# Performance work log

Measured on AMD Instinct MI355X. Metric: run time of the kernel, lower is better.

## Reference

```python
import jax, jax.numpy as jnp
import numpy as np

ALPHA = 0.2  # leaky-relu negative slope AND the residual scale self.alpha

def setup_inputs() -> dict:
    key = jax.random.key(0)
    k1, k2, k3 = jax.random.split(key, 3)
    B, N, C_in, C_out = 8, 2048, 128, 128
    text = jax.random.normal(k1, (B, N, C_in), dtype=jnp.float32)
    adj = jnp.ones((B, N, N), dtype=jnp.float32)  # unused by the layer's forward
    W = jax.random.normal(k2, (C_in, C_out), dtype=jnp.float32) * (1.414 / np.sqrt(C_in + C_out))
    a = jax.random.normal(k3, (2 * C_out, 1), dtype=jnp.float32) * (1.414 / np.sqrt(2 * C_out + 1))
    return {"text": text, "adj": adj, "W": W, "a": a}

def reference(text, adj, W, a):
    # text: [B,N,C_in]; adj is unused (faithful to the source forward).
    h = jnp.einsum('bnc,cf->bnf', text, W)                  # [B,N,F]
    F_out = W.shape[1]
    a1 = a[:F_out, 0]                                       # score contribution of node i
    a2 = a[F_out:, 0]                                       # score contribution of node j
    s1 = jnp.einsum('bnf,f->bn', h, a1)                     # [B,N]
    s2 = jnp.einsum('bnf,f->bn', h, a2)                     # [B,N]
    # leakyrelu(cat(h_i,h_j) @ a) == leakyrelu(s1_i + s2_j): avoids O(N^2*2F) concat
    e = jax.nn.leaky_relu(s1[:, :, None] + s2[:, None, :], negative_slope=ALPHA)  # [B,N,N]
    attention = jax.nn.softmax(e, axis=2)                   # dropout is a no-op in eval mode
    h_prime = jnp.einsum('bij,bjf->bif', attention, h)      # [B,N,F]
    return jax.nn.elu(h_prime + ALPHA * h)
```

## Files before the change

kernel.cpp:

```cpp
#include <hip/hip_runtime.h>
#include <hip/hip_bf16.h>
#include <math.h>

#define LRELU_ALPHA 0.2f

constexpr int B_ = 8;
constexpr int N_ = 2048;
constexpr int M_ = B_ * N_;
constexpr int SEG = 32;
constexpr int NSEG = N_ / SEG;

__global__ __launch_bounds__(256) void k_gemm(const float* __restrict__ text,
                                              const float* __restrict__ W,
                                              const float* __restrict__ a,
                                              float* __restrict__ h,
                                              float* __restrict__ s1,
                                              float* __restrict__ s2,
                                              float* __restrict__ eN0,
                                              float* __restrict__ eP0) {
    __shared__ __align__(16) float As[64 * 132];

    const int tid = threadIdx.x;
    const int r0  = blockIdx.x * 64;
    const int cx  = tid & 15;
    const int ry  = tid >> 4;
    const int c0  = cx * 4;
    const int c1  = 64 + cx * 4;
    const int rr0 = ry * 4;

    for (int idx = tid; idx < 64 * 32; idx += 256) {
        int r = idx >> 5, k4 = (idx & 31) * 4;
        *(float4*)&As[r * 132 + k4] =
            *(const float4*)&text[(size_t)(r0 + r) * 128 + k4];
    }
    __syncthreads();

    float acc[4][8];
#pragma unroll
    for (int i = 0; i < 4; ++i)
#pragma unroll
        for (int j = 0; j < 8; ++j) acc[i][j] = 0.f;

#pragma unroll 2
    for (int k0 = 0; k0 < 128; k0 += 4) {
        float4 av[4];
#pragma unroll
        for (int i = 0; i < 4; ++i)
            av[i] = *(const float4*)&As[(rr0 + i) * 132 + k0];
#pragma unroll
        for (int kk = 0; kk < 4; ++kk) {
            float4 w0 = *(const float4*)&W[(size_t)(k0 + kk) * 128 + c0];
            float4 w1 = *(const float4*)&W[(size_t)(k0 + kk) * 128 + c1];
#pragma unroll
            for (int i = 0; i < 4; ++i) {
                const float avv = (kk == 0) ? av[i].x : (kk == 1) ? av[i].y
                                : (kk == 2) ? av[i].z : av[i].w;
                acc[i][0] += avv * w0.x; acc[i][1] += avv * w0.y;
                acc[i][2] += avv * w0.z; acc[i][3] += avv * w0.w;
                acc[i][4] += avv * w1.x; acc[i][5] += avv * w1.y;
                acc[i][6] += avv * w1.z; acc[i][7] += avv * w1.w;
            }
        }
    }

    float4 a1lo = *(const float4*)&a[c0];
    float4 a1hi = *(const float4*)&a[c1];
    float4 a2lo = *(const float4*)&a[128 + c0];
    float4 a2hi = *(const float4*)&a[128 + c1];

#pragma unroll
    for (int i = 0; i < 4; ++i) {
        const int row = r0 + rr0 + i;
        float4 o0 = {acc[i][0], acc[i][1], acc[i][2], acc[i][3]};
        float4 o1 = {acc[i][4], acc[i][5], acc[i][6], acc[i][7]};
        *(float4*)&h[(size_t)row * 128 + c0] = o0;
        *(float4*)&h[(size_t)row * 128 + c1] = o1;

        float p1 = o0.x*a1lo.x + o0.y*a1lo.y + o0.z*a1lo.z + o0.w*a1lo.w
                 + o1.x*a1hi.x + o1.y*a1hi.y + o1.z*a1hi.z + o1.w*a1hi.w;
        float p2 = o0.x*a2lo.x + o0.y*a2lo.y + o0.z*a2lo.z + o0.w*a2lo.w
                 + o1.x*a2hi.x + o1.y*a2hi.y + o1.z*a2hi.z + o1.w*a2hi.w;
#pragma unroll
        for (int off = 8; off >= 1; off >>= 1) {
            p1 += __shfl_xor(p1, off);
            p2 += __shfl_xor(p2, off);
        }
        if (cx == 0) {
            s1[row] = p1;
            s2[row] = p2;
            eN0[row] = expf(LRELU_ALPHA * p2);
            eP0[row] = expf(p2);
        }
    }
}

__global__ __launch_bounds__(512) void k_rank(const float* __restrict__ s2,
                                              const float* __restrict__ eN0,
                                              const float* __restrict__ eP0,
                                              const float* __restrict__ s1,
                                              int* __restrict__ perm,
                                              float* __restrict__ eNs,
                                              float* __restrict__ ePs,
                                              int* __restrict__ rank,
                                              float* __restrict__ ZN,
                                              float* __restrict__ ZP) {
    __shared__ float ls2[2048], leN[2048], leP[2048];
    __shared__ int   redc[512], redm[512];
    __shared__ float redn[512], redp[512];

    const int b  = blockIdx.x >> 5;
    const int eb = blockIdx.x & 31;
    const int tid = threadIdx.x;
    const int e = tid & 63;
    const int c = tid >> 6;

    {
        const float4* g2 = (const float4*)(s2  + b * 2048);
        const float4* gn = (const float4*)(eN0 + b * 2048);
        const float4* gp = (const float4*)(eP0 + b * 2048);
        ((float4*)ls2)[tid] = g2[tid];
        ((float4*)leN)[tid] = gn[tid];
        ((float4*)leP)[tid] = gp[tid];
    }
    __syncthreads();

    const int i  = eb * 64 + e;
    const int gi = b * 2048 + i;
    const float myS2 = ls2[i];
    const float thr  = -s1[gi];

    int cnt = 0, mr = 0;
    float sn = 0.f, sp = 0.f;
    const int j0 = c * 256;
#pragma unroll 4
    for (int j = j0; j < j0 + 256; j += 4) {
        float4 v  = *(const float4*)&ls2[j];
        float4 en = *(const float4*)&leN[j];
        float4 ep = *(const float4*)&leP[j];
#define PROC(vv, ee, pp, jj)                                             \
        { bool le = (vv) <= thr;                                         \
          cnt += le ? 1 : 0;                                             \
          sn  += le ? (ee) : 0.f;                                        \
          sp  += le ? 0.f : (pp);                                        \
          mr  += ((vv) < myS2 || ((vv) == myS2 && (jj) < i)) ? 1 : 0; }
        PROC(v.x, en.x, ep.x, j + 0)
        PROC(v.y, en.y, ep.y, j + 1)
        PROC(v.z, en.z, ep.z, j + 2)
        PROC(v.w, en.w, ep.w, j + 3)
#undef PROC
    }
    redc[tid] = cnt; redm[tid] = mr; redn[tid] = sn; redp[tid] = sp;
    __syncthreads();
    if (c == 0) {
        int tc = 0, tm = 0; float tn = 0.f, tp = 0.f;
#pragma unroll
        for (int cc = 0; cc < 8; ++cc) {
            tc += redc[cc * 64 + e];
            tm += redm[cc * 64 + e];
            tn += redn[cc * 64 + e];
            tp += redp[cc * 64 + e];
        }
        perm[b * 2048 + tm] = i;
        eNs [b * 2048 + tm] = leN[i];
        ePs [b * 2048 + tm] = leP[i];
        rank[gi] = tc;
        ZN[gi] = tn;
        ZP[gi] = tp;
    }
}

__global__ __launch_bounds__(128) void k_segsum(const float* __restrict__ h,
                                                const int* __restrict__ perm,
                                                const float* __restrict__ eNs,
                                                const float* __restrict__ ePs,
                                                float* __restrict__ segN,
                                                float* __restrict__ segP) {
    const int blk = blockIdx.x;
    const int b = blk >> 6, s = blk & 63;
    const int f = threadIdx.x;
    const int rbase = s * SEG;
    float an = 0.f, ap = 0.f;
#pragma unroll 4
    for (int r = 0; r < SEG; ++r) {
        int rr = b * 2048 + rbase + r;
        float hv = h[(size_t)(b * 2048 + perm[rr]) * 128 + f];
        an += eNs[rr] * hv;
        ap += ePs[rr] * hv;
    }
    segN[blk * 128 + f] = an;
    segP[blk * 128 + f] = ap;
}

__global__ __launch_bounds__(128) void k_prefix(const float* __restrict__ h,
                                                const int* __restrict__ perm,
                                                const float* __restrict__ eNs,
                                                const float* __restrict__ ePs,
                                                const float* __restrict__ segN,
                                                const float* __restrict__ segP,
                                                __hip_bfloat16* __restrict__ Pre,
                                                __hip_bfloat16* __restrict__ Suf) {
    const int blk  = blockIdx.x;
    const int dir  = blk & 1;
    const int task = blk >> 1;
    const int b = task >> 6, s = task & 63;
    const int f = threadIdx.x;
    const int rbase = s * SEG;

    if (dir == 0) {
        float an = 0.f;
        for (int ss = 0; ss < s; ++ss) an += segN[(b * NSEG + ss) * 128 + f];
#pragma unroll 4
        for (int r = 0; r < SEG; ++r) {
            int rr = b * 2048 + rbase + r;
            Pre[(size_t)(b * 2049 + rbase + r) * 128 + f] = __float2bfloat16(an);
            an += eNs[rr] * h[(size_t)(b * 2048 + perm[rr]) * 128 + f];
        }
        if (s == NSEG - 1)
            Pre[(size_t)(b * 2049 + 2048) * 128 + f] = __float2bfloat16(an);
    } else {
        float ap = 0.f;
        for (int ss = s + 1; ss < NSEG; ++ss) ap += segP[(b * NSEG + ss) * 128 + f];
#pragma unroll 4
        for (int r = SEG - 1; r >= 0; --r) {
            int rr = b * 2048 + rbase + r;
            ap += ePs[rr] * h[(size_t)(b * 2048 + perm[rr]) * 128 + f];
            Suf[(size_t)(b * 2049 + rbase + r) * 128 + f] = __float2bfloat16(ap);
        }
        if (s == NSEG - 1)
            Suf[(size_t)(b * 2049 + 2048) * 128 + f] = __float2bfloat16(0.f);
    }
}

__global__ __launch_bounds__(256) void k_out(const float* __restrict__ h,
                                             const float* __restrict__ s1,
                                             const int* __restrict__ rank,
                                             const float* __restrict__ ZN,
                                             const float* __restrict__ ZP,
                                             const __hip_bfloat16* __restrict__ Pre,
                                             const __hip_bfloat16* __restrict__ Suf,
                                             float* __restrict__ out) {
    const int tid = threadIdx.x;
    const int lr = tid >> 7, f = tid & 127;
    const int i = blockIdx.x * 2 + lr;
    const int b = i >> 11;

    const float s1v = s1[i];
    const float E1 = expf(s1v);
    const float E2 = expf(LRELU_ALPHA * s1v);
    const int   r  = rank[i];
    const float Z  = E1 * ZP[i] + E2 * ZN[i];
    const size_t o = (size_t)(b * 2049 + r) * 128 + f;
    const float hp = (E1 * __bfloat162float(Suf[o]) + E2 * __bfloat162float(Pre[o])) / Z;
    const float x = hp + LRELU_ALPHA * h[(size_t)i * 128 + f];
    out[(size_t)i * 128 + f] = (x > 0.f) ? x : expm1f(x);
}

extern "C" void kernel_launch(void* const* d_in, const int* in_sizes, int n_in,
                              void* d_out, int out_size, void* d_ws, size_t ws_size,
                              hipStream_t stream) {
    const float* text = (const float*)d_in[0];
    const float* W = (const float*)d_in[2];
    const float* a = (const float*)d_in[3];
    float* out = (float*)d_out;

    float* p = (float*)d_ws;
    float* h    = p; p += (size_t)M_ * 128;
    float* s1   = p; p += M_;
    float* s2   = p; p += M_;
    float* eN0  = p; p += M_;
    float* eP0  = p; p += M_;
    int*   perm = (int*)p; p += M_;
    float* eNs  = p; p += M_;
    float* ePs  = p; p += M_;
    int*   rank = (int*)p; p += M_;
    float* ZN   = p; p += M_;
    float* ZP   = p; p += M_;
    float* segN = p; p += B_ * NSEG * 128;
    float* segP = p; p += B_ * NSEG * 128;
    __hip_bfloat16* Pre = (__hip_bfloat16*)p; p += (size_t)B_ * 2049 * 128 / 2;
    __hip_bfloat16* Suf = (__hip_bfloat16*)p; p += (size_t)B_ * 2049 * 128 / 2;

    hipLaunchKernelGGL(k_gemm,   dim3(M_ / 64),       dim3(256), 0, stream,
                       text, W, a, h, s1, s2, eN0, eP0);
    hipLaunchKernelGGL(k_rank,   dim3(B_ * 32),       dim3(512), 0, stream,
                       s2, eN0, eP0, s1, perm, eNs, ePs, rank, ZN, ZP);
    hipLaunchKernelGGL(k_segsum, dim3(B_ * NSEG),     dim3(128), 0, stream,
                       h, perm, eNs, ePs, segN, segP);
    hipLaunchKernelGGL(k_prefix, dim3(B_ * NSEG * 2), dim3(128), 0, stream,
                       h, perm, eNs, ePs, segN, segP, Pre, Suf);
    hipLaunchKernelGGL(k_out,    dim3(M_ / 2),        dim3(256), 0, stream,
                       h, s1, rank, ZN, ZP, Pre, Suf, out);
}
```

Baseline: 267.7 us.

## Fuse prefix scan and output into bucketed per-segment kernel, stage W in LDS

Merges the prefix/suffix scan and output kernels into one kernel per segment. It keeps the scanned prefix and suffix rows in shared memory instead of writing bf16 Pre/Suf arrays to global memory. Nodes are bucketed by rank segment with atomics in the rank kernel so each block can emit the outputs whose rank falls in its segment. The GEMM now stages W in LDS, and the h gathers in segsum and scan are hoisted into registers. Risks include a serial per-bucket output loop with uneven bucket sizes, and extra LDS use in the GEMM that may lower occupancy.

```diff
diff --git a/kernel.cpp b/kernel.cpp
--- a/kernel.cpp
+++ b/kernel.cpp
@@ -17,11 +17,18 @@
                                               float* __restrict__ s1,
                                               float* __restrict__ s2,
                                               float* __restrict__ eN0,
-                                              float* __restrict__ eP0) {
+                                              float* __restrict__ eP0,
+                                              int* __restrict__ bcnt) {
     __shared__ __align__(16) float As[64 * 132];
+    __shared__ __align__(16) float Ws[128 * 128];
 
     const int tid = threadIdx.x;
-    const int r0  = blockIdx.x * 64;
+    const int blk = blockIdx.x;
+
+    if (blk == 0)
+        for (int t = tid; t < B_ * NSEG; t += 256) bcnt[t] = 0;
+
+    const int r0  = blk * 64;
     const int cx  = tid & 15;
     const int ry  = tid >> 4;
     const int c0  = cx * 4;
@@ -33,6 +40,10 @@
         *(float4*)&As[r * 132 + k4] =
             *(const float4*)&text[(size_t)(r0 + r) * 128 + k4];
     }
+    for (int idx = tid; idx < 128 * 32; idx += 256) {
+        int k = idx >> 5, f4 = (idx & 31) * 4;
+        *(float4*)&Ws[k * 128 + f4] = *(const float4*)&W[(size_t)k * 128 + f4];
+    }
     __syncthreads();
 
     float acc[4][8];
@@ -49,8 +60,8 @@
             av[i] = *(const float4*)&As[(rr0 + i) * 132 + k0];
 #pragma unroll
         for (int kk = 0; kk < 4; ++kk) {
-            float4 w0 = *(const float4*)&W[(size_t)(k0 + kk) * 128 + c0];
-            float4 w1 = *(const float4*)&W[(size_t)(k0 + kk) * 128 + c1];
+            float4 w0 = *(const float4*)&Ws[(k0 + kk) * 128 + c0];
+            float4 w1 = *(const float4*)&Ws[(k0 + kk) * 128 + c1];
 #pragma unroll
             for (int i = 0; i < 4; ++i) {
                 const float avv = (kk == 0) ? av[i].x : (kk == 1) ? av[i].y
@@ -101,9 +112,10 @@
                                               int* __restrict__ perm,
                                               float* __restrict__ eNs,
                                               float* __restrict__ ePs,
-                                              int* __restrict__ rank,
                                               float* __restrict__ ZN,
-                                              float* __restrict__ ZP) {
+                                              float* __restrict__ ZP,
+                                              int* __restrict__ bcnt,
+                                              int* __restrict__ bucket) {
     __shared__ float ls2[2048], leN[2048], leP[2048];
     __shared__ int   redc[512], redm[512];
     __shared__ float redn[512], redp[512];
@@ -163,9 +175,12 @@
         perm[b * 2048 + tm] = i;
         eNs [b * 2048 + tm] = leN[i];
         ePs [b * 2048 + tm] = leP[i];
-        rank[gi] = tc;
         ZN[gi] = tn;
         ZP[gi] = tp;
+        const int seg = min(tc >> 5, NSEG - 1);
+        const int pos = atomicAdd(&bcnt[b * NSEG + seg], 1);
+        if (pos < 2048)
+            bucket[(b * NSEG + seg) * 2048 + pos] = i | (tc << 11);
     }
 }
 
@@ -178,81 +193,87 @@
     const int blk = blockIdx.x;
     const int b = blk >> 6, s = blk & 63;
     const int f = threadIdx.x;
-    const int rbase = s * SEG;
+    const int rr0 = b * 2048 + s * SEG;
+
+    int pm[SEG];
+#pragma unroll
+    for (int r = 0; r < SEG; ++r) pm[r] = perm[rr0 + r];
+    float hv[SEG];
+#pragma unroll
+    for (int r = 0; r < SEG; ++r)
+        hv[r] = h[(size_t)(b * 2048 + pm[r]) * 128 + f];
+
     float an = 0.f, ap = 0.f;
-#pragma unroll 4
+#pragma unroll
     for (int r = 0; r < SEG; ++r) {
-        int rr = b * 2048 + rbase + r;
-        float hv = h[(size_t)(b * 2048 + perm[rr]) * 128 + f];
-        an += eNs[rr] * hv;
-        ap += ePs[rr] * hv;
+        an += eNs[rr0 + r] * hv[r];
+        ap += ePs[rr0 + r] * hv[r];
     }
     segN[blk * 128 + f] = an;
     segP[blk * 128 + f] = ap;
 }
 
-__global__ __launch_bounds__(128) void k_prefix(const float* __restrict__ h,
-                                                const int* __restrict__ perm,
-                                                const float* __restrict__ eNs,
-                                                const float* __restrict__ ePs,
-                                                const float* __restrict__ segN,
-                                                const float* __restrict__ segP,
-                                                __hip_bfloat16* __restrict__ Pre,
-                                                __hip_bfloat16* __restrict__ Suf) {
-    const int blk  = blockIdx.x;
-    const int dir  = blk & 1;
-    const int task = blk >> 1;
-    const int b = task >> 6, s = task & 63;
+__global__ __launch_bounds__(128) void k_scanout(
+    const float* __restrict__ h, const int* __restrict__ perm,
+    const float* __restrict__ eNs, const float* __restrict__ ePs,
+    const float* __restrict__ s1,
+    const float* __restrict__ ZN, const float* __restrict__ ZP,
+    const float* __restrict__ segN, const float* __restrict__ segP,
+    const int* __restrict__ bcnt, const int* __restrict__ bucket,
+    float* __restrict__ out) {
+
+    __shared__ float anL[(SEG + 1) * 128];
+    __shared__ float apL[(SEG + 1) * 128];
+
+    const int blk = blockIdx.x;
+    const int b = blk >> 6, s = blk & 63;
     const int f = threadIdx.x;
-    const int rbase = s * SEG;
-
-    if (dir == 0) {
-        float an = 0.f;
-        for (int ss = 0; ss < s; ++ss) an += segN[(b * NSEG + ss) * 128 + f];
-#pragma unroll 4
-        for (int r = 0; r < SEG; ++r) {
-            int rr = b * 2048 + rbase + r;
-            Pre[(size_t)(b * 2049 + rbase + r) * 128 + f] = __float2bfloat16(an);
-            an += eNs[rr] * h[(size_t)(b * 2048 + perm[rr]) * 128 + f];
-        }
-        if (s == NSEG - 1)
-            Pre[(size_t)(b * 2049 + 2048) * 128 + f] = __float2bfloat16(an);
-    } else {
-        float ap = 0.f;
-        for (int ss = s + 1; ss < NSEG; ++ss) ap += segP[(b * NSEG + ss) * 128 + f];
-#pragma unroll 4
-        for (int r = SEG - 1; r >= 0; --r) {
-            int rr = b * 2048 + rbase + r;
-            ap += ePs[rr] * h[(size_t)(b * 2048 + perm[rr]) * 128 + f];
-            Suf[(size_t)(b * 2049 + rbase + r) * 128 + f] = __float2bfloat16(ap);
-        }
-        if (s == NSEG - 1)
-            Suf[(size_t)(b * 2049 + 2048) * 128 + f] = __float2bfloat16(0.f);
-    }
-}
-
-__global__ __launch_bounds__(256) void k_out(const float* __restrict__ h,
-                                             const float* __restrict__ s1,
-                                             const int* __restrict__ rank,
-                                             const float* __restrict__ ZN,
-                                             const float* __restrict__ ZP,
-                                             const __hip_bfloat16* __restrict__ Pre,
-                                             const __hip_bfloat16* __restrict__ Suf,
-                                             float* __restrict__ out) {
-    const int tid = threadIdx.x;
-    const int lr = tid >> 7, f = tid & 127;
-    const int i = blockIdx.x * 2 + lr;
-    const int b = i >> 11;
-
-    const float s1v = s1[i];
-    const float E1 = expf(s1v);
-    const float E2 = expf(LRELU_ALPHA * s1v);
-    const int   r  = rank[i];
-    const float Z  = E1 * ZP[i] + E2 * ZN[i];
-    const size_t o = (size_t)(b * 2049 + r) * 128 + f;
-    const float hp = (E1 * __bfloat162float(Suf[o]) + E2 * __bfloat162float(Pre[o])) / Z;
-    const float x = hp + LRELU_ALPHA * h[(size_t)i * 128 + f];
-    out[(size_t)i * 128 + f] = (x > 0.f) ? x : expm1f(x);
+
+    float bn = 0.f, bp = 0.f;
+    for (int ss = 0; ss < s; ++ss)        bn += segN[(b * NSEG + ss) * 128 + f];
+    for (int ss = s + 1; ss < NSEG; ++ss) bp += segP[(b * NSEG + ss) * 128 + f];
+
+    const int rr0 = b * 2048 + s * SEG;
+    int pm[SEG];
+#pragma unroll
+    for (int r = 0; r < SEG; ++r) pm[r] = perm[rr0 + r];
+    float hv[SEG];
+#pragma unroll
+    for (int r = 0; r < SEG; ++r)
+        hv[r] = h[(size_t)(b * 2048 + pm[r]) * 128 + f];
+
+    float an = bn;
+#pragma unroll
+    for (int r = 0; r < SEG; ++r) {
+        anL[r * 128 + f] = an;
+        an += eNs[rr0 + r] * hv[r];
+    }
+    anL[SEG * 128 + f] = an;
+
+    float ap = bp;
+    apL[SEG * 128 + f] = ap;
+#pragma unroll
+    for (int r = SEG - 1; r >= 0; --r) {
+        ap += ePs[rr0 + r] * hv[r];
+        apL[r * 128 + f] = ap;
+    }
+    __syncthreads();
+
+    const int m = min(bcnt[b * NSEG + s], 2048);
+    for (int t = 0; t < m; ++t) {
+        const int packed = bucket[(b * NSEG + s) * 2048 + t];
+        const int il = packed & 2047;
+        const int tc = packed >> 11;
+        const int gi = b * 2048 + il;
+        const int pl = tc - s * SEG;
+        const float s1v = s1[gi];
+        const float E1 = expf(s1v);
+        const float E2 = expf(LRELU_ALPHA * s1v);
+        const float Z  = E1 * ZP[gi] + E2 * ZN[gi];
+        const float hp = (E1 * apL[pl * 128 + f] + E2 * anL[pl * 128 + f]) / Z;
+        const float x  = hp + LRELU_ALPHA * h[(size_t)gi * 128 + f];
+        out[(size_t)gi * 128 + f] = (x > 0.f) ? x : expm1f(x);
+    }
 }
 
 extern "C" void kernel_launch(void* const* d_in, const int* in_sizes, int n_in,
@@ -272,22 +293,20 @@
     int*   perm = (int*)p; p += M_;
     float* eNs  = p; p += M_;
     float* ePs  = p; p += M_;
-    int*   rank = (int*)p; p += M_;
     float* ZN   = p; p += M_;
     float* ZP   = p; p += M_;
     float* segN = p; p += B_ * NSEG * 128;
     float* segP = p; p += B_ * NSEG * 128;
-    __hip_bfloat16* Pre = (__hip_bfloat16*)p; p += (size_t)B_ * 2049 * 128 / 2;
-    __hip_bfloat16* Suf = (__hip_bfloat16*)p; p += (size_t)B_ * 2049 * 128 / 2;
-
-    hipLaunchKernelGGL(k_gemm,   dim3(M_ / 64),       dim3(256), 0, stream,
-                       text, W, a, h, s1, s2, eN0, eP0);
-    hipLaunchKernelGGL(k_rank,   dim3(B_ * 32),       dim3(512), 0, stream,
-                       s2, eN0, eP0, s1, perm, eNs, ePs, rank, ZN, ZP);
-    hipLaunchKernelGGL(k_segsum, dim3(B_ * NSEG),     dim3(128), 0, stream,
+    int*   bcnt = (int*)p; p += B_ * NSEG;
+    int*   bucket = (int*)p; p += (size_t)B_ * NSEG * 2048;
+
+    hipLaunchKernelGGL(k_gemm,   dim3(M_ / 64),   dim3(256), 0, stream,
+                       text, W, a, h, s1, s2, eN0, eP0, bcnt);
+    hipLaunchKernelGGL(k_rank,   dim3(B_ * 32),   dim3(512), 0, stream,
+                       s2, eN0, eP0, s1, perm, eNs, ePs, ZN, ZP, bcnt, bucket);
+    hipLaunchKernelGGL(k_segsum, dim3(B_ * NSEG), dim3(128), 0, stream,
                        h, perm, eNs, ePs, segN, segP);
-    hipLaunchKernelGGL(k_prefix, dim3(B_ * NSEG * 2), dim3(128), 0, stream,
-                       h, perm, eNs, ePs, segN, segP, Pre, Suf);
-    hipLaunchKernelGGL(k_out,    dim3(M_ / 2),        dim3(256), 0, stream,
-                       h, s1, rank, ZN, ZP, Pre, Suf, out);
-}
+    hipLaunchKernelGGL(k_scanout, dim3(B_ * NSEG), dim3(128), 0, stream,
+                       h, perm, eNs, ePs, s1, ZN, ZP, segN, segP,
+                       bcnt, bucket, out);
+}
```

New measurement: 244.5 us. 8.7% less time.
